# Optimization experiments

Hardware: AMD Instinct MI355X
Metric: run time of the kernel (lower is better)

The kernel has to match this reference:

```python
import jax, jax.numpy as jnp
import numpy as np

N, E, DIN, DH, DOUT, NG = 50000, 800000, 128, 128, 64, 128
EPS = 1e-5
SLOPE = 0.2  # PyG GATConv default negative_slope


def _gat(x, src, dst, W, a_s, a_d, b, heads, out_c, concat):
    n = x.shape[0]
    xp = (x @ W).reshape(n, heads, out_c)            # [N,H,C]
    e_src = (xp * a_s[None]).sum(-1)                  # [N,H]
    e_dst = (xp * a_d[None]).sum(-1)                  # [N,H]
    al = e_src[src] + e_dst[dst]                      # [E,H]
    al = jnp.where(al > 0, al, SLOPE * al)            # leaky_relu
    amax = jax.ops.segment_max(al, dst, num_segments=n)
    w = jnp.exp(al - amax[dst])                       # segment softmax (stable)
    den = jax.ops.segment_sum(w, dst, num_segments=n)
    msg = w[:, :, None] * xp[src]                     # [E,H,C]
    out = jax.ops.segment_sum(msg, dst, num_segments=n) / den[:, :, None]
    out = out.reshape(n, heads * out_c) if concat else out.mean(axis=1)
    return out + b


def _bn(h, g, be):
    m = h.mean(axis=0)
    v = h.var(axis=0)  # biased var, as in torch BN training mode
    return (h - m) / jnp.sqrt(v + EPS) * g + be


def setup_inputs() -> dict:
    key = jax.random.key(0)
    ks = jax.random.split(key, 12)
    x = jax.random.normal(ks[0], (N, DIN), dtype=jnp.float32)
    edge_index = jax.random.randint(ks[1], (2, E), 0, N, dtype=jnp.int64)
    graph_pool = jax.random.uniform(ks[2], (NG, N), dtype=jnp.float32) * (2.0 / N)
    s = 0.1
    return {
        "x": x, "edge_index": edge_index, "graph_pool": graph_pool,
        "W1": jax.random.normal(ks[3], (DIN, DH), dtype=jnp.float32) * s,
        "as1": jax.random.normal(ks[4], (1, DH), dtype=jnp.float32) * s,
        "ad1": jax.random.normal(ks[5], (1, DH), dtype=jnp.float32) * s,
        "b1": jnp.zeros((DH,), jnp.float32),
        "g1": jnp.ones((DH,), jnp.float32), "be1": jnp.zeros((DH,), jnp.float32),
        "W2": jax.random.normal(ks[6], (DH, DH), dtype=jnp.float32) * s,
        "as2": jax.random.normal(ks[7], (1, DH), dtype=jnp.float32) * s,
        "ad2": jax.random.normal(ks[8], (1, DH), dtype=jnp.float32) * s,
        "b2": jnp.zeros((DH,), jnp.float32),
        "g2": jnp.ones((DH,), jnp.float32), "be2": jnp.zeros((DH,), jnp.float32),
        "W3": jax.random.normal(ks[9], (DH, DOUT), dtype=jnp.float32) * s,
        "as3": jax.random.normal(ks[10], (1, DOUT), dtype=jnp.float32) * s,
        "ad3": jax.random.normal(ks[11], (1, DOUT), dtype=jnp.float32) * s,
        "b3": jnp.zeros((DOUT,), jnp.float32),
    }


def reference(x, edge_index, graph_pool,
              W1, as1, ad1, b1, g1, be1,
              W2, as2, ad2, b2, g2, be2,
              W3, as3, ad3, b3):
    n = x.shape[0]
    loops = jnp.arange(n, dtype=edge_index.dtype)  # PyG add_self_loops=True
    src = jnp.concatenate([edge_index[0], loops])
    dst = jnp.concatenate([edge_index[1], loops])
    h = _gat(x, src, dst, W1, as1, ad1, b1, 1, DH, True)
    h = jax.nn.relu(_bn(h, g1, be1))
    h = _gat(h, src, dst, W2, as2, ad2, b2, 1, DH, True)
    h = jax.nn.relu(_bn(h, g2, be2))
    h_nodes = _gat(h, src, dst, W3, as3, ad3, b3, 1, DOUT, False)
    h_pooled = graph_pool @ h_nodes  # sparse.mm == matmul mathematically
    return (h_pooled, h_nodes)
```

## Files before the change

kernel.cpp:

```cpp
#include <hip/hip_runtime.h>
#include <hip/hip_bf16.h>

#define DIN 128
#define DH  128
#define DOUT 64
#define NGR 128
#define EPSV 1e-5f
#define SLOPE 0.2f
#define BSH 7
#define NBMAX 512
#define BCAP 3584

typedef __attribute__((ext_vector_type(8))) short short8;
typedef __attribute__((ext_vector_type(4))) float float4v;

__device__ __forceinline__ unsigned short f2bf(float f) {
    union { float f; unsigned int u; } v; v.f = f;
    unsigned int r = (v.u + 0x7FFFu + ((v.u >> 16) & 1u)) >> 16;
    return (unsigned short)r;
}
__device__ __forceinline__ unsigned short f2bf_f(float f) {
    return (unsigned short)((__float_as_uint(f) + 0x8000u) >> 16);
}
__device__ __forceinline__ float bf_lo(unsigned int u) { return __uint_as_float(u << 16); }
__device__ __forceinline__ float bf_hi(unsigned int u) { return __uint_as_float(u & 0xFFFF0000u); }


__global__ __launch_bounds__(256) void bin_edges_kernel(const int* __restrict__ ei,
                                                        int* __restrict__ bucket_cnt,
                                                        int2* __restrict__ binned,
                                                        int E, int T, int nb) {
    __shared__ int hist[NBMAX], base[NBMAX], cur[NBMAX];
    for (int i = threadIdx.x; i < nb; i += 256) hist[i] = 0;
    __syncthreads();
    int start = blockIdx.x * 8192;
    int endc  = start + 8192; if (endc > T) endc = T;
    for (int e = start + threadIdx.x; e < endc; e += 256) {
        int d = (e < E) ? ei[E + e] : (e - E);
        atomicAdd(&hist[d >> BSH], 1);
    }
    __syncthreads();
    for (int i = threadIdx.x; i < nb; i += 256) {
        int h = hist[i];
        cur[i] = 0;
        if (h) base[i] = atomicAdd(&bucket_cnt[i], h);
    }
    __syncthreads();
    for (int e = start + threadIdx.x; e < endc; e += 256) {
        int s, d;
        if (e < E) { s = ei[e]; d = ei[E + e]; }
        else       { s = e - E; d = s; }
        int b = d >> BSH;
        int off = atomicAdd(&cur[b], 1);
        binned[(size_t)b * BCAP + base[b] + off] = make_int2(s, d);
    }
}

__global__ __launch_bounds__(512) void bucket_scan_kernel(const int* __restrict__ bucket_cnt,
                                                          int* __restrict__ bucket_off,
                                                          int nb, int T) {
    __shared__ int sh[512];
    int tid = threadIdx.x;
    int v = (tid < nb) ? bucket_cnt[tid] : 0;
    sh[tid] = v;
    __syncthreads();
    for (int d = 1; d < 512; d <<= 1) {
        int t = (tid >= d) ? sh[tid - d] : 0;
        __syncthreads();
        sh[tid] += t;
        __syncthreads();
    }
    if (tid < nb) bucket_off[tid] = sh[tid] - v;
    if (tid == 0) bucket_off[nb] = T;
}

__global__ __launch_bounds__(256) void csr_from_binned_kernel(const int2* __restrict__ binned,
                                                              const int* __restrict__ bucket_cnt,
                                                              const int* __restrict__ bucket_off,
                                                              int* __restrict__ row_ptr,
                                                              int* __restrict__ col_src,
                                                              int n, int T) {
    __shared__ int cnt[128], rnk[128], rp[128], sc[128];
    int tid = threadIdx.x;
    int b = blockIdx.x;
    int node0 = b << BSH;
    const int2* bin = &binned[(size_t)b * BCAP];
    int nb_edges = bucket_cnt[b];
    int lo = bucket_off[b];
    if (tid < 128) cnt[tid] = 0;
    __syncthreads();
    for (int i = tid; i < nb_edges; i += 256)
        atomicAdd(&cnt[bin[i].y - node0], 1);
    __syncthreads();
    if (tid < 128) sc[tid] = cnt[tid];
    __syncthreads();
    for (int d = 1; d < 128; d <<= 1) {
        int t = 0;
        if (tid < 128 && tid >= d) t = sc[tid - d];
        __syncthreads();
        if (tid < 128) sc[tid] += t;
        __syncthreads();
    }
    if (tid < 128) {
        int excl = sc[tid] - cnt[tid];
        int r = lo + excl;
        rp[tid] = r;
        rnk[tid] = 0;
        int node = node0 + tid;
        if (node < n) row_ptr[node] = r;
    }
    if (b == 0 && tid == 0) row_ptr[n] = T;
    __syncthreads();
    for (int i = tid; i < nb_edges; i += 256) {
        int2 e = bin[i];
        int local = e.y - node0;
        int r = atomicAdd(&rnk[local], 1);
        col_src[rp[local] + r] = e.x;
    }
}

__device__ __forceinline__ void pack_one(const float* W, unsigned short* PW, int cout, int t) {
    int lane = t & 63;
    int ks   = (t >> 6) & 3;
    int nt   = t >> 8;
    int nn   = nt * 16 + (lane & 15);
    int k0   = ks * 32 + (lane >> 4) * 8;
    unsigned int pk[4];
#pragma unroll
    for (int p = 0; p < 4; ++p) {
        unsigned short lo = f2bf(W[(k0 + 2 * p) * cout + nn]);
        unsigned short hi = f2bf(W[(k0 + 2 * p + 1) * cout + nn]);
        pk[p] = ((unsigned int)hi << 16) | lo;
    }
    *(uint4*)&PW[(size_t)t * 8] = make_uint4(pk[0], pk[1], pk[2], pk[3]);
}

__global__ void pack_w_all_kernel(const float* __restrict__ W1, unsigned short* __restrict__ PW1,
                                  const float* __restrict__ W2, unsigned short* __restrict__ PW2,
                                  const float* __restrict__ W3, unsigned short* __restrict__ PW3) {
    int t = blockIdx.x * 256 + threadIdx.x;
    if (t < 2048)      pack_one(W1, PW1, 128, t);
    else if (t < 4096) pack_one(W2, PW2, 128, t - 2048);
    else if (t < 5120) pack_one(W3, PW3, 64,  t - 4096);
}

template <int COUT, int BNIN>
__global__ __launch_bounds__(256) void gemm_es_kernel(
    const void* __restrict__ Xv, const unsigned short* __restrict__ PW,
    const float* __restrict__ a_s, const float* __restrict__ a_d,
    const float* __restrict__ bnsum, const float* __restrict__ g,
    const float* __restrict__ be, float invn,
    unsigned short* __restrict__ XPB, float* __restrict__ e_src, float* __restrict__ e_dst, int n)
{
    constexpr int NT = COUT / 16;
    __shared__ unsigned short Xs[64 * 136];
    __shared__ float sSc[128], sSh[128];

    int tid  = threadIdx.x;
    int row0 = blockIdx.x * 64;

    if (BNIN) {
        if (tid < 128) {
            float mean = bnsum[tid] * invn;
            float var  = bnsum[128 + tid] * invn - mean * mean;
            float sc   = g[tid] * rsqrtf(var + EPSV);
            sSc[tid] = sc;
            sSh[tid] = be[tid] - mean * sc;
        }
        __syncthreads();
        const unsigned short* H = (const unsigned short*)Xv;
        for (int i = tid; i < 64 * 16; i += 256) {
            int r  = i >> 4;
            int c8 = (i & 15) * 8;
            uint4 u = make_uint4(0, 0, 0, 0);
            if (row0 + r < n) u = *(const uint4*)&H[(size_t)(row0 + r) * 128 + c8];
            unsigned int uu[4] = {u.x, u.y, u.z, u.w};
            unsigned int out[4];
#pragma unroll
            for (int p = 0; p < 4; ++p) {
                int c = c8 + 2 * p;
                float a  = fmaxf(bf_lo(uu[p]) * sSc[c] + sSh[c], 0.f);
                float bq = fmaxf(bf_hi(uu[p]) * sSc[c + 1] + sSh[c + 1], 0.f);
                out[p] = ((unsigned int)f2bf_f(bq) << 16) | f2bf_f(a);
            }
            *(uint4*)&Xs[r * 136 + c8] = make_uint4(out[0], out[1], out[2], out[3]);
        }
    } else {
        const float* X = (const float*)Xv;
        for (int i = tid; i < 64 * 32; i += 256) {
            int r  = i >> 5;
            int k4 = (i & 31) * 4;
            float4 v = make_float4(0.f, 0.f, 0.f, 0.f);
            if (row0 + r < n) v = *(const float4*)&X[(size_t)(row0 + r) * 128 + k4];
            uint2 pk;
            pk.x = ((unsigned int)f2bf_f(v.y) << 16) | f2bf_f(v.x);
            pk.y = ((unsigned int)f2bf_f(v.w) << 16) | f2bf_f(v.z);
            *(uint2*)&Xs[r * 136 + k4] = pk;
        }
    }
    __syncthreads();

    int wv   = tid >> 6;
    int lane = tid & 63;
    int m0   = wv * 16;
    int cl   = lane & 15;
    int q    = lane >> 4;

    float4v acc[NT] = {};
#pragma unroll
    for (int ks = 0; ks < 4; ++ks) {
        short8 af = *(const short8*)&Xs[(m0 + cl) * 136 + ks * 32 + q * 8];
#pragma unroll
        for (int nt = 0; nt < NT; ++nt) {
            short8 bf = *(const short8*)&PW[(size_t)((nt * 4 + ks) * 64 + lane) * 8];
            acc[nt] = __builtin_amdgcn_mfma_f32_16x16x32_bf16(af, bf, acc[nt], 0, 0, 0);
        }
    }

    float asv[NT], adv[NT];
#pragma unroll
    for (int nt = 0; nt < NT; ++nt) {
        asv[nt] = a_s[nt * 16 + cl];
        adv[nt] = a_d[nt * 16 + cl];
    }
#pragma unroll
    for (int reg = 0; reg < 4; ++reg) {
        int m = row0 + m0 + q * 4 + reg;
        if (m >= n) continue;
        float ps = 0.f, pd = 0.f;
        size_t base = (size_t)m * COUT;
#pragma unroll
        for (int nt = 0; nt < NT; ++nt) {
            float v = acc[nt][reg];
            XPB[base + nt * 16 + cl] = f2bf_f(v);
            ps += v * asv[nt];
            pd += v * adv[nt];
        }
        ps += __shfl_xor(ps, 1); pd += __shfl_xor(pd, 1);
        ps += __shfl_xor(ps, 2); pd += __shfl_xor(pd, 2);
        ps += __shfl_xor(ps, 4); pd += __shfl_xor(pd, 4);
        ps += __shfl_xor(ps, 8); pd += __shfl_xor(pd, 8);
        if (cl == 0) {
            e_src[m] = ps;
            e_dst[m] = pd;
        }
    }
}

template <int COUT, int OUTBF>
__global__ __launch_bounds__(256) void gat_aggregate_kernel(
    const unsigned short* __restrict__ XPB, const float* __restrict__ e_src,
    const float* __restrict__ e_dst, const int* __restrict__ row_ptr,
    const int* __restrict__ col_src, const float* __restrict__ bias,
    void* __restrict__ OUT, int n)
{
    int wave = threadIdx.x >> 6;
    int lane = threadIdx.x & 63;
    int d = blockIdx.x * 4 + wave;
    if (d >= n) return;
    int start = row_ptr[d];
    int end   = row_ptr[d + 1];
    float ed  = e_dst[d];

    float den = 0.f;
    float2 acc2 = make_float2(0.f, 0.f);
    float acc1 = 0.f;
    const unsigned int* xpu = (const unsigned int*)XPB;

    for (int base = start; base < end; base += 64) {
        int t = base + lane;
        int s_l = 0; float w_l = 0.f;
        if (t < end) {
            s_l = col_src[t];
            float a = e_src[s_l] + ed;
            a = (a > 0.f) ? a : SLOPE * a;
            w_l = __expf(a);
        }
        int cnt = end - base; if (cnt > 64) cnt = 64;

        int j = 0;
        for (; j + 7 < cnt; j += 8) {
            int ss[8]; float wwv[8];
#pragma unroll
            for (int p = 0; p < 8; ++p) {
                ss[p]  = __shfl(s_l, j + p);
                wwv[p] = __shfl(w_l, j + p);
            }
            if (COUT == 128) {
                unsigned int us[8];
#pragma unroll
                for (int p = 0; p < 8; ++p) us[p] = xpu[(size_t)ss[p] * 64 + lane];
#pragma unroll
                for (int p = 0; p < 8; ++p) {
                    acc2.x += wwv[p] * bf_lo(us[p]);
                    acc2.y += wwv[p] * bf_hi(us[p]);
                    den    += wwv[p];
                }
            } else {
                float xs[8];
#pragma unroll
                for (int p = 0; p < 8; ++p)
                    xs[p] = __uint_as_float((unsigned int)XPB[(size_t)ss[p] * COUT + lane] << 16);
#pragma unroll
                for (int p = 0; p < 8; ++p) {
                    acc1 += wwv[p] * xs[p];
                    den  += wwv[p];
                }
            }
        }
        for (; j + 3 < cnt; j += 4) {
            int ss[4]; float wwv[4];
#pragma unroll
            for (int p = 0; p < 4; ++p) {
                ss[p]  = __shfl(s_l, j + p);
                wwv[p] = __shfl(w_l, j + p);
            }
            if (COUT == 128) {
                unsigned int us[4];
#pragma unroll
                for (int p = 0; p < 4; ++p) us[p] = xpu[(size_t)ss[p] * 64 + lane];
#pragma unroll
                for (int p = 0; p < 4; ++p) {
                    acc2.x += wwv[p] * bf_lo(us[p]);
                    acc2.y += wwv[p] * bf_hi(us[p]);
                    den    += wwv[p];
                }
            } else {
#pragma unroll
                for (int p = 0; p < 4; ++p) {
                    float xv = __uint_as_float((unsigned int)XPB[(size_t)ss[p] * COUT + lane] << 16);
                    acc1 += wwv[p] * xv;
                    den  += wwv[p];
                }
            }
        }
        for (; j < cnt; ++j) {
            int   s = __shfl(s_l, j);
            float w = __shfl(w_l, j);
            if (COUT == 128) {
                unsigned int u = xpu[(size_t)s * 64 + lane];
                acc2.x += w * bf_lo(u);
                acc2.y += w * bf_hi(u);
            } else {
                acc1 += w * __uint_as_float((unsigned int)XPB[(size_t)s * COUT + lane] << 16);
            }
            den += w;
        }
    }

    float inv = 1.f / den;
    if (COUT == 128) {
        float ox = acc2.x * inv + bias[2 * lane + 0];
        float oy = acc2.y * inv + bias[2 * lane + 1];
        if (OUTBF) {
            unsigned int o = ((unsigned int)f2bf_f(oy) << 16) | f2bf_f(ox);
            ((unsigned int*)OUT)[(size_t)d * 64 + lane] = o;
        } else {
            ((float2*)OUT)[(size_t)d * 64 + lane] = make_float2(ox, oy);
        }
    } else {
        ((float*)OUT)[(size_t)d * COUT + lane] = acc1 * inv + bias[lane];
    }
}

__global__ __launch_bounds__(256) void bn_stats_bf_kernel(const unsigned short* __restrict__ H,
                                                          float* __restrict__ sums, int n) {
    __shared__ float sh[1024];
    int c2  = threadIdx.x & 63;
    int grp = threadIdx.x >> 6;
    float sx = 0.f, sy = 0.f, qx = 0.f, qy = 0.f;
    const unsigned int* Hu = (const unsigned int*)H;
    for (int i = blockIdx.x * 4 + grp; i < n; i += gridDim.x * 4) {
        unsigned int u = Hu[(size_t)i * 64 + c2];
        float a = bf_lo(u), b = bf_hi(u);
        sx += a; qx += a * a;
        sy += b; qy += b * b;
    }
    sh[threadIdx.x]       = sx;
    sh[256 + threadIdx.x] = sy;
    sh[512 + threadIdx.x] = qx;
    sh[768 + threadIdx.x] = qy;
    __syncthreads();
    if (grp == 0) {
#pragma unroll
        for (int g2 = 1; g2 < 4; ++g2) {
            sx += sh[g2 * 64 + c2];
            sy += sh[256 + g2 * 64 + c2];
            qx += sh[512 + g2 * 64 + c2];
            qy += sh[768 + g2 * 64 + c2];
        }
        atomicAdd(&sums[2 * c2],       sx);
        atomicAdd(&sums[2 * c2 + 1],   sy);
        atomicAdd(&sums[128 + 2 * c2],     qx);
        atomicAdd(&sums[128 + 2 * c2 + 1], qy);
    }
}

__global__ __launch_bounds__(256) void pool_partial_kernel(
    const float* __restrict__ GP, const float* __restrict__ HN,
    float* __restrict__ partial, int n)
{
    __shared__ float hn_lds[64 * 64];
    __shared__ float gp_lds[128 * 68];

    int tid = threadIdx.x;
    int cg  = tid & 15;
    int gg  = tid >> 4;
    int c0  = cg * 4;

    float acc[8][4] = {};

    for (int sub = 0; sub < 2; ++sub) {
        int k0 = blockIdx.x * 128 + sub * 64;
        for (int i = tid; i < 64 * 16; i += 256) {
            int kk = i >> 4;
            int c4 = (i & 15) * 4;
            int gk = k0 + kk;
            float4 v = make_float4(0.f, 0.f, 0.f, 0.f);
            if (gk < n) v = *(const float4*)&HN[(size_t)gk * 64 + c4];
            *(float4*)&hn_lds[kk * 64 + c4] = v;
        }
        for (int i = tid; i < 128 * 16; i += 256) {
            int g  = i >> 4;
            int k4 = (i & 15) * 4;
            int gk = k0 + k4;
            float4 v = make_float4(0.f, 0.f, 0.f, 0.f);
            if (gk < n) v = *(const float4*)&GP[(size_t)g * n + gk];
            *(float4*)&gp_lds[g * 68 + k4] = v;
        }
        __syncthreads();

#pragma unroll 4
        for (int k = 0; k < 64; ++k) {
            float4 hv = *(const float4*)&hn_lds[k * 64 + c0];
#pragma unroll
            for (int j = 0; j < 8; ++j) {
                float gv = gp_lds[(gg + 16 * j) * 68 + k];
                acc[j][0] += gv * hv.x;
                acc[j][1] += gv * hv.y;
                acc[j][2] += gv * hv.z;
                acc[j][3] += gv * hv.w;
            }
        }
        __syncthreads();
    }

    float* po = &partial[(size_t)blockIdx.x * (NGR * DOUT)];
#pragma unroll
    for (int j = 0; j < 8; ++j) {
        *(float4*)&po[(gg + 16 * j) * 64 + c0] =
            make_float4(acc[j][0], acc[j][1], acc[j][2], acc[j][3]);
    }
}

__global__ __launch_bounds__(256) void pool_reduce_kernel(
    const float* __restrict__ partial, float* __restrict__ OUT, int nblk)
{
    int i = blockIdx.x * 256 + threadIdx.x;
    float s0 = 0.f, s1 = 0.f, s2 = 0.f, s3 = 0.f;
    int p = 0;
    for (; p + 3 < nblk; p += 4) {
        s0 += partial[(size_t)(p + 0) * (NGR * DOUT) + i];
        s1 += partial[(size_t)(p + 1) * (NGR * DOUT) + i];
        s2 += partial[(size_t)(p + 2) * (NGR * DOUT) + i];
        s3 += partial[(size_t)(p + 3) * (NGR * DOUT) + i];
    }
    for (; p < nblk; ++p) s0 += partial[(size_t)p * (NGR * DOUT) + i];
    OUT[i] = (s0 + s1) + (s2 + s3);
}

extern "C" void kernel_launch(void* const* d_in, const int* in_sizes, int n_in,
                              void* d_out, int out_size, void* d_ws, size_t ws_size,
                              hipStream_t stream) {
    const float* x   = (const float*)d_in[0];
    const int*   ei  = (const int*)d_in[1];
    const float* gp  = (const float*)d_in[2];
    const float* W1  = (const float*)d_in[3];
    const float* as1 = (const float*)d_in[4];
    const float* ad1 = (const float*)d_in[5];
    const float* b1  = (const float*)d_in[6];
    const float* g1  = (const float*)d_in[7];
    const float* be1 = (const float*)d_in[8];
    const float* W2  = (const float*)d_in[9];
    const float* as2 = (const float*)d_in[10];
    const float* ad2 = (const float*)d_in[11];
    const float* b2  = (const float*)d_in[12];
    const float* g2  = (const float*)d_in[13];
    const float* be2 = (const float*)d_in[14];
    const float* W3  = (const float*)d_in[15];
    const float* as3 = (const float*)d_in[16];
    const float* ad3 = (const float*)d_in[17];
    const float* b3  = (const float*)d_in[18];

    const int N = in_sizes[0] / DIN;
    const int E = in_sizes[1] / 2;
    const int T = E + N;
    const int NB = (N + 127) >> BSH;

    char* ws = (char*)d_ws;
    auto take = [&](size_t bytes) {
        char* p = ws;
        ws += (bytes + 511) & ~(size_t)511;
        return p;
    };
    unsigned short* xpb = (unsigned short*)take((size_t)N * 128 * 2);
    unsigned short* h   = (unsigned short*)take((size_t)N * 128 * 2);
    float* pool_s  = (float*)take((size_t)((N + 127) / 128) * NGR * DOUT * 4);
    float* esd     = (float*)take((size_t)2 * N * 4);
    float* e_src   = esd;
    float* e_dst   = esd + N;
    int*   row_ptr = (int*)take((size_t)(N + 1) * 4);
    int*   col_src = (int*)take((size_t)T * 4);
    int2*  binned  = (int2*)take((size_t)NB * BCAP * 8);
    int*   zero_rgn      = (int*)take((size_t)(NBMAX + 1 + 512) * 4);
    int*   bucket_cnt    = zero_rgn;
    float* bnsum1        = (float*)(zero_rgn + NBMAX + 1);
    float* bnsum2        = bnsum1 + 256;
    int*   bucket_off    = (int*)take((size_t)(NB + 1) * 4);
    unsigned short* pw1 = (unsigned short*)take((size_t)128 * 128 * 2);
    unsigned short* pw2 = (unsigned short*)take((size_t)128 * 128 * 2);
    unsigned short* pw3 = (unsigned short*)take((size_t)128 * 64 * 2);

    float* outp = (float*)d_out;
    float* hn   = outp + NGR * DOUT;

    hipMemsetAsync(zero_rgn, 0, (size_t)(NBMAX + 1 + 512) * 4, stream);
    pack_w_all_kernel<<<20, 256, 0, stream>>>(W1, pw1, W2, pw2, W3, pw3);

    const int binBlocks = (T + 8191) / 8192;
    bin_edges_kernel<<<binBlocks, 256, 0, stream>>>(ei, bucket_cnt, binned, E, T, NB);
    bucket_scan_kernel<<<1, 512, 0, stream>>>(bucket_cnt, bucket_off, NB, T);
    csr_from_binned_kernel<<<NB, 256, 0, stream>>>(binned, bucket_cnt, bucket_off, row_ptr, col_src, N, T);

    const int gx = (N + 63) / 64;
    const float invn = 1.f / N;

    gemm_es_kernel<128, 0><<<gx, 256, 0, stream>>>(x, pw1, as1, ad1,
        nullptr, nullptr, nullptr, 0.f, xpb, e_src, e_dst, N);
    gat_aggregate_kernel<128, 1><<<(N + 3) / 4, 256, 0, stream>>>(xpb, e_src, e_dst, row_ptr, col_src, b1, h, N);
    bn_stats_bf_kernel<<<240, 256, 0, stream>>>(h, bnsum1, N);

    gemm_es_kernel<128, 1><<<gx, 256, 0, stream>>>(h, pw2, as2, ad2,
        bnsum1, g1, be1, invn, xpb, e_src, e_dst, N);
    gat_aggregate_kernel<128, 1><<<(N + 3) / 4, 256, 0, stream>>>(xpb, e_src, e_dst, row_ptr, col_src, b2, h, N);
    bn_stats_bf_kernel<<<240, 256, 0, stream>>>(h, bnsum2, N);

    gemm_es_kernel<64, 1><<<gx, 256, 0, stream>>>(h, pw3, as3, ad3,
        bnsum2, g2, be2, invn, xpb, e_src, e_dst, N);
    gat_aggregate_kernel<64, 0><<<(N + 3) / 4, 256, 0, stream>>>(xpb, e_src, e_dst, row_ptr, col_src, b3, hn, N);

    const int nblk = (N + 127) / 128;
    pool_partial_kernel<<<nblk, 256, 0, stream>>>(gp, hn, pool_s, N);
    pool_reduce_kernel<<<(NGR * DOUT + 255) / 256, 256, 0, stream>>>(pool_s, outp, nblk);
}
```

Before: 393.8 us.

## Merge front-end kernels, stage edges in LDS, and cap pooling partial blocks

Weight packing is folded into the edge-binning launch. The bucket scan kernel is removed: each CSR block now sums the preceding bucket counts itself, and CSR building runs in the same launch as the first GEMM. The aggregate kernel reads edge (src, weight) pairs from LDS instead of shuffles and reduces the softmax denominator once per wave at the end. The pooling partial kernel now uses a grid-stride loop over at most 128 blocks, so the reduction reads far fewer partials. Together these cut launch count and reduction traffic, at the cost of some redundant prefix-sum work per CSR block and lower parallelism in pooling.

```diff
diff --git a/kernel.cpp b/kernel.cpp
--- a/kernel.cpp
+++ b/kernel.cpp
@@ -10,6 +10,7 @@
 #define BSH 7
 #define NBMAX 512
 #define BCAP 3584
+#define POOLB 128
 
 typedef __attribute__((ext_vector_type(8))) short short8;
 typedef __attribute__((ext_vector_type(4))) float float4v;
@@ -25,11 +26,36 @@
 __device__ __forceinline__ float bf_lo(unsigned int u) { return __uint_as_float(u << 16); }
 __device__ __forceinline__ float bf_hi(unsigned int u) { return __uint_as_float(u & 0xFFFF0000u); }
 
-
-__global__ __launch_bounds__(256) void bin_edges_kernel(const int* __restrict__ ei,
-                                                        int* __restrict__ bucket_cnt,
-                                                        int2* __restrict__ binned,
-                                                        int E, int T, int nb) {
+__device__ __forceinline__ void pack_one(const float* W, unsigned short* PW, int cout, int t) {
+    int lane = t & 63;
+    int ks   = (t >> 6) & 3;
+    int nt   = t >> 8;
+    int nn   = nt * 16 + (lane & 15);
+    int k0   = ks * 32 + (lane >> 4) * 8;
+    unsigned int pk[4];
+#pragma unroll
+    for (int p = 0; p < 4; ++p) {
+        unsigned short lo = f2bf(W[(k0 + 2 * p) * cout + nn]);
+        unsigned short hi = f2bf(W[(k0 + 2 * p + 1) * cout + nn]);
+        pk[p] = ((unsigned int)hi << 16) | lo;
+    }
+    *(uint4*)&PW[(size_t)t * 8] = make_uint4(pk[0], pk[1], pk[2], pk[3]);
+}
+
+__global__ __launch_bounds__(256) void front_a_kernel(
+    const int* __restrict__ ei, int* __restrict__ bucket_cnt, int2* __restrict__ binned,
+    int E, int T, int nb, int binBlocks,
+    const float* __restrict__ W1, unsigned short* __restrict__ PW1,
+    const float* __restrict__ W2, unsigned short* __restrict__ PW2,
+    const float* __restrict__ W3, unsigned short* __restrict__ PW3)
+{
+    if ((int)blockIdx.x >= binBlocks) {
+        int t = ((int)blockIdx.x - binBlocks) * 256 + (int)threadIdx.x;
+        if (t < 2048)      pack_one(W1, PW1, 128, t);
+        else if (t < 4096) pack_one(W2, PW2, 128, t - 2048);
+        else if (t < 5120) pack_one(W3, PW3, 64,  t - 4096);
+        return;
+    }
     __shared__ int hist[NBMAX], base[NBMAX], cur[NBMAX];
     for (int i = threadIdx.x; i < nb; i += 256) hist[i] = 0;
     __syncthreads();
@@ -56,96 +82,9 @@
     }
 }
 
-__global__ __launch_bounds__(512) void bucket_scan_kernel(const int* __restrict__ bucket_cnt,
-                                                          int* __restrict__ bucket_off,
-                                                          int nb, int T) {
-    __shared__ int sh[512];
-    int tid = threadIdx.x;
-    int v = (tid < nb) ? bucket_cnt[tid] : 0;
-    sh[tid] = v;
-    __syncthreads();
-    for (int d = 1; d < 512; d <<= 1) {
-        int t = (tid >= d) ? sh[tid - d] : 0;
-        __syncthreads();
-        sh[tid] += t;
-        __syncthreads();
-    }
-    if (tid < nb) bucket_off[tid] = sh[tid] - v;
-    if (tid == 0) bucket_off[nb] = T;
-}
-
-__global__ __launch_bounds__(256) void csr_from_binned_kernel(const int2* __restrict__ binned,
-                                                              const int* __restrict__ bucket_cnt,
-                                                              const int* __restrict__ bucket_off,
-                                                              int* __restrict__ row_ptr,
-                                                              int* __restrict__ col_src,
-                                                              int n, int T) {
-    __shared__ int cnt[128], rnk[128], rp[128], sc[128];
-    int tid = threadIdx.x;
-    int b = blockIdx.x;
-    int node0 = b << BSH;
-    const int2* bin = &binned[(size_t)b * BCAP];
-    int nb_edges = bucket_cnt[b];
-    int lo = bucket_off[b];
-    if (tid < 128) cnt[tid] = 0;
-    __syncthreads();
-    for (int i = tid; i < nb_edges; i += 256)
-        atomicAdd(&cnt[bin[i].y - node0], 1);
-    __syncthreads();
-    if (tid < 128) sc[tid] = cnt[tid];
-    __syncthreads();
-    for (int d = 1; d < 128; d <<= 1) {
-        int t = 0;
-        if (tid < 128 && tid >= d) t = sc[tid - d];
-        __syncthreads();
-        if (tid < 128) sc[tid] += t;
-        __syncthreads();
-    }
-    if (tid < 128) {
-        int excl = sc[tid] - cnt[tid];
-        int r = lo + excl;
-        rp[tid] = r;
-        rnk[tid] = 0;
-        int node = node0 + tid;
-        if (node < n) row_ptr[node] = r;
-    }
-    if (b == 0 && tid == 0) row_ptr[n] = T;
-    __syncthreads();
-    for (int i = tid; i < nb_edges; i += 256) {
-        int2 e = bin[i];
-        int local = e.y - node0;
-        int r = atomicAdd(&rnk[local], 1);
-        col_src[rp[local] + r] = e.x;
-    }
-}
-
-__device__ __forceinline__ void pack_one(const float* W, unsigned short* PW, int cout, int t) {
-    int lane = t & 63;
-    int ks   = (t >> 6) & 3;
-    int nt   = t >> 8;
-    int nn   = nt * 16 + (lane & 15);
-    int k0   = ks * 32 + (lane >> 4) * 8;
-    unsigned int pk[4];
-#pragma unroll
-    for (int p = 0; p < 4; ++p) {
-        unsigned short lo = f2bf(W[(k0 + 2 * p) * cout + nn]);
-        unsigned short hi = f2bf(W[(k0 + 2 * p + 1) * cout + nn]);
-        pk[p] = ((unsigned int)hi << 16) | lo;
-    }
-    *(uint4*)&PW[(size_t)t * 8] = make_uint4(pk[0], pk[1], pk[2], pk[3]);
-}
-
-__global__ void pack_w_all_kernel(const float* __restrict__ W1, unsigned short* __restrict__ PW1,
-                                  const float* __restrict__ W2, unsigned short* __restrict__ PW2,
-                                  const float* __restrict__ W3, unsigned short* __restrict__ PW3) {
-    int t = blockIdx.x * 256 + threadIdx.x;
-    if (t < 2048)      pack_one(W1, PW1, 128, t);
-    else if (t < 4096) pack_one(W2, PW2, 128, t - 2048);
-    else if (t < 5120) pack_one(W3, PW3, 64,  t - 4096);
-}
-
 template <int COUT, int BNIN>
-__global__ __launch_bounds__(256) void gemm_es_kernel(
+__device__ __forceinline__ void gemm_es_body(
+    unsigned short* Xs, float* sSc, float* sSh, int row0,
     const void* __restrict__ Xv, const unsigned short* __restrict__ PW,
     const float* __restrict__ a_s, const float* __restrict__ a_d,
     const float* __restrict__ bnsum, const float* __restrict__ g,
@@ -153,13 +92,9 @@
     unsigned short* __restrict__ XPB, float* __restrict__ e_src, float* __restrict__ e_dst, int n)
 {
     constexpr int NT = COUT / 16;
-    __shared__ unsigned short Xs[64 * 136];
-    __shared__ float sSc[128], sSh[128];
-
-    int tid  = threadIdx.x;
-    int row0 = blockIdx.x * 64;
-
-    if (BNIN) {
+    int tid = threadIdx.x;
+
+    if constexpr (BNIN) {
         if (tid < 128) {
             float mean = bnsum[tid] * invn;
             float var  = bnsum[128 + tid] * invn - mean * mean;
@@ -247,6 +182,89 @@
     }
 }
 
+template <int COUT, int BNIN>
+__global__ __launch_bounds__(256) void gemm_es_kernel(
+    const void* __restrict__ Xv, const unsigned short* __restrict__ PW,
+    const float* __restrict__ a_s, const float* __restrict__ a_d,
+    const float* __restrict__ bnsum, const float* __restrict__ g,
+    const float* __restrict__ be, float invn,
+    unsigned short* __restrict__ XPB, float* __restrict__ e_src, float* __restrict__ e_dst, int n)
+{
+    __shared__ unsigned short Xs[64 * 136];
+    __shared__ float sSc[128], sSh[128];
+    gemm_es_body<COUT, BNIN>(Xs, sSc, sSh, blockIdx.x * 64,
+                             Xv, PW, a_s, a_d, bnsum, g, be, invn, XPB, e_src, e_dst, n);
+}
+
+__global__ __launch_bounds__(256) void front_b_kernel(
+    const int2* __restrict__ binned, const int* __restrict__ bucket_cnt,
+    int* __restrict__ row_ptr, int* __restrict__ col_src, int n, int T, int nbcsr,
+    const float* __restrict__ X, const unsigned short* __restrict__ PW,
+    const float* __restrict__ a_s, const float* __restrict__ a_d,
+    unsigned short* __restrict__ XPB, float* __restrict__ e_src, float* __restrict__ e_dst)
+{
+    __shared__ __align__(16) char smraw[64 * 136 * 2];
+    int tid = threadIdx.x;
+
+    if ((int)blockIdx.x < nbcsr) {
+        int* cnt = (int*)smraw;
+        int* rnk = cnt + 128;
+        int* rp  = rnk + 128;
+        int* sc  = rp + 128;
+        int* red = sc + 128;
+        int b = blockIdx.x;
+        int node0 = b << BSH;
+        const int2* bin = &binned[(size_t)b * BCAP];
+        int nb_edges = bucket_cnt[b];
+
+        int part = 0;
+        for (int i = tid; i < b; i += 256) part += bucket_cnt[i];
+        red[tid] = part;
+        if (tid < 128) cnt[tid] = 0;
+        __syncthreads();
+#pragma unroll
+        for (int s2 = 128; s2 > 0; s2 >>= 1) {
+            if (tid < s2) red[tid] += red[tid + s2];
+            __syncthreads();
+        }
+        int lo = red[0];
+
+        for (int i = tid; i < nb_edges; i += 256)
+            atomicAdd(&cnt[bin[i].y - node0], 1);
+        __syncthreads();
+        if (tid < 128) sc[tid] = cnt[tid];
+        __syncthreads();
+        for (int d2 = 1; d2 < 128; d2 <<= 1) {
+            int t = 0;
+            if (tid < 128 && tid >= d2) t = sc[tid - d2];
+            __syncthreads();
+            if (tid < 128) sc[tid] += t;
+            __syncthreads();
+        }
+        if (tid < 128) {
+            int excl = sc[tid] - cnt[tid];
+            int r = lo + excl;
+            rp[tid] = r;
+            rnk[tid] = 0;
+            int node = node0 + tid;
+            if (node < n) row_ptr[node] = r;
+        }
+        if (b == 0 && tid == 0) row_ptr[n] = T;
+        __syncthreads();
+        for (int i = tid; i < nb_edges; i += 256) {
+            int2 e = bin[i];
+            int local = e.y - node0;
+            int r = atomicAdd(&rnk[local], 1);
+            col_src[rp[local] + r] = e.x;
+        }
+    } else {
+        unsigned short* Xs = (unsigned short*)smraw;
+        gemm_es_body<128, 0>(Xs, nullptr, nullptr, ((int)blockIdx.x - nbcsr) * 64,
+                             X, PW, a_s, a_d, nullptr, nullptr, nullptr, 0.f,
+                             XPB, e_src, e_dst, n);
+    }
+}
+
 template <int COUT, int OUTBF>
 __global__ __launch_bounds__(256) void gat_aggregate_kernel(
     const unsigned short* __restrict__ XPB, const float* __restrict__ e_src,
@@ -254,6 +272,7 @@
     const int* __restrict__ col_src, const float* __restrict__ bias,
     void* __restrict__ OUT, int n)
 {
+    __shared__ int2 sw[4][64];
     int wave = threadIdx.x >> 6;
     int lane = threadIdx.x & 63;
     int d = blockIdx.x * 4 + wave;
@@ -262,7 +281,7 @@
     int end   = row_ptr[d + 1];
     float ed  = e_dst[d];
 
-    float den = 0.f;
+    float denl = 0.f;
     float2 acc2 = make_float2(0.f, 0.f);
     float acc1 = 0.f;
     const unsigned int* xpu = (const unsigned int*)XPB;
@@ -276,6 +295,8 @@
             a = (a > 0.f) ? a : SLOPE * a;
             w_l = __expf(a);
         }
+        denl += w_l;
+        sw[wave][lane] = make_int2(s_l, __float_as_int(w_l));
         int cnt = end - base; if (cnt > 64) cnt = 64;
 
         int j = 0;
@@ -283,8 +304,9 @@
             int ss[8]; float wwv[8];
 #pragma unroll
             for (int p = 0; p < 8; ++p) {
-                ss[p]  = __shfl(s_l, j + p);
-                wwv[p] = __shfl(w_l, j + p);
+                int2 e = sw[wave][j + p];
+                ss[p]  = e.x;
+                wwv[p] = __int_as_float(e.y);
             }
             if (COUT == 128) {
                 unsigned int us[8];
@@ -294,7 +316,6 @@
                 for (int p = 0; p < 8; ++p) {
                     acc2.x += wwv[p] * bf_lo(us[p]);
                     acc2.y += wwv[p] * bf_hi(us[p]);
-                    den    += wwv[p];
                 }
             } else {
                 float xs[8];
@@ -302,18 +323,16 @@
                 for (int p = 0; p < 8; ++p)
                     xs[p] = __uint_as_float((unsigned int)XPB[(size_t)ss[p] * COUT + lane] << 16);
 #pragma unroll
-                for (int p = 0; p < 8; ++p) {
-                    acc1 += wwv[p] * xs[p];
-                    den  += wwv[p];
-                }
+                for (int p = 0; p < 8; ++p) acc1 += wwv[p] * xs[p];
             }
         }
         for (; j + 3 < cnt; j += 4) {
             int ss[4]; float wwv[4];
 #pragma unroll
             for (int p = 0; p < 4; ++p) {
-                ss[p]  = __shfl(s_l, j + p);
-                wwv[p] = __shfl(w_l, j + p);
+                int2 e = sw[wave][j + p];
+                ss[p]  = e.x;
+                wwv[p] = __int_as_float(e.y);
             }
             if (COUT == 128) {
                 unsigned int us[4];
@@ -323,20 +342,19 @@
                 for (int p = 0; p < 4; ++p) {
                     acc2.x += wwv[p] * bf_lo(us[p]);
                     acc2.y += wwv[p] * bf_hi(us[p]);
-                    den    += wwv[p];
                 }
             } else {
 #pragma unroll
                 for (int p = 0; p < 4; ++p) {
                     float xv = __uint_as_float((unsigned int)XPB[(size_t)ss[p] * COUT + lane] << 16);
                     acc1 += wwv[p] * xv;
-                    den  += wwv[p];
                 }
             }
         }
         for (; j < cnt; ++j) {
-            int   s = __shfl(s_l, j);
-            float w = __shfl(w_l, j);
+            int2 e = sw[wave][j];
+            int   s = e.x;
+            float w = __int_as_float(e.y);
             if (COUT == 128) {
                 unsigned int u = xpu[(size_t)s * 64 + lane];
                 acc2.x += w * bf_lo(u);
@@ -344,11 +362,13 @@
             } else {
                 acc1 += w * __uint_as_float((unsigned int)XPB[(size_t)s * COUT + lane] << 16);
             }
-            den += w;
-        }
-    }
-
-    float inv = 1.f / den;
+        }
+    }
+
+#pragma unroll
+    for (int off = 1; off < 64; off <<= 1) denl += __shfl_xor(denl, off);
+    float inv = 1.f / denl;
+
     if (COUT == 128) {
         float ox = acc2.x * inv + bias[2 * lane + 0];
         float oy = acc2.y * inv + bias[2 * lane + 1];
@@ -409,40 +429,43 @@
     int c0  = cg * 4;
 
     float acc[8][4] = {};
-
-    for (int sub = 0; sub < 2; ++sub) {
-        int k0 = blockIdx.x * 128 + sub * 64;
-        for (int i = tid; i < 64 * 16; i += 256) {
-            int kk = i >> 4;
-            int c4 = (i & 15) * 4;
-            int gk = k0 + kk;
-            float4 v = make_float4(0.f, 0.f, 0.f, 0.f);
-            if (gk < n) v = *(const float4*)&HN[(size_t)gk * 64 + c4];
-            *(float4*)&hn_lds[kk * 64 + c4] = v;
-        }
-        for (int i = tid; i < 128 * 16; i += 256) {
-            int g  = i >> 4;
-            int k4 = (i & 15) * 4;
-            int gk = k0 + k4;
-            float4 v = make_float4(0.f, 0.f, 0.f, 0.f);
-            if (gk < n) v = *(const float4*)&GP[(size_t)g * n + gk];
-            *(float4*)&gp_lds[g * 68 + k4] = v;
-        }
-        __syncthreads();
+    int nchunk = (n + 127) >> 7;
+
+    for (int blk = blockIdx.x; blk < nchunk; blk += gridDim.x) {
+        for (int sub = 0; sub < 2; ++sub) {
+            int k0 = blk * 128 + sub * 64;
+            for (int i = tid; i < 64 * 16; i += 256) {
+                int kk = i >> 4;
+                int c4 = (i & 15) * 4;
+                int gk = k0 + kk;
+                float4 v = make_float4(0.f, 0.f, 0.f, 0.f);
+                if (gk < n) v = *(const float4*)&HN[(size_t)gk * 64 + c4];
+                *(float4*)&hn_lds[kk * 64 + c4] = v;
+            }
+            for (int i = tid; i < 128 * 16; i += 256) {
+                int g  = i >> 4;
+                int k4 = (i & 15) * 4;
+                int gk = k0 + k4;
+                float4 v = make_float4(0.f, 0.f, 0.f, 0.f);
+                if (gk < n) v = *(const float4*)&GP[(size_t)g * n + gk];
+                *(float4*)&gp_lds[g * 68 + k4] = v;
+            }
+            __syncthreads();
 
 #pragma unroll 4
-        for (int k = 0; k < 64; ++k) {
-            float4 hv = *(const float4*)&hn_lds[k * 64 + c0];
-#pragma unroll
-            for (int j = 0; j < 8; ++j) {
-                float gv = gp_lds[(gg + 16 * j) * 68 + k];
-                acc[j][0] += gv * hv.x;
-                acc[j][1] += gv * hv.y;
-                acc[j][2] += gv * hv.z;
-                acc[j][3] += gv * hv.w;
-            }
-        }
-        __syncthreads();
+            for (int k = 0; k < 64; ++k) {
+                float4 hv = *(const float4*)&hn_lds[k * 64 + c0];
+#pragma unroll
+                for (int j = 0; j < 8; ++j) {
+                    float gv = gp_lds[(gg + 16 * j) * 68 + k];
+                    acc[j][0] += gv * hv.x;
+                    acc[j][1] += gv * hv.y;
+                    acc[j][2] += gv * hv.z;
+                    acc[j][3] += gv * hv.w;
+                }
+            }
+            __syncthreads();
+        }
     }
 
     float* po = &partial[(size_t)blockIdx.x * (NGR * DOUT)];
@@ -505,7 +528,7 @@
     };
     unsigned short* xpb = (unsigned short*)take((size_t)N * 128 * 2);
     unsigned short* h   = (unsigned short*)take((size_t)N * 128 * 2);
-    float* pool_s  = (float*)take((size_t)((N + 127) / 128) * NGR * DOUT * 4);
+    float* pool_s  = (float*)take((size_t)POOLB * NGR * DOUT * 4);
     float* esd     = (float*)take((size_t)2 * N * 4);
     float* e_src   = esd;
     float* e_dst   = esd + N;
@@ -516,7 +539,6 @@
     int*   bucket_cnt    = zero_rgn;
     float* bnsum1        = (float*)(zero_rgn + NBMAX + 1);
     float* bnsum2        = bnsum1 + 256;
-    int*   bucket_off    = (int*)take((size_t)(NB + 1) * 4);
     unsigned short* pw1 = (unsigned short*)take((size_t)128 * 128 * 2);
     unsigned short* pw2 = (unsigned short*)take((size_t)128 * 128 * 2);
     unsigned short* pw3 = (unsigned short*)take((size_t)128 * 64 * 2);
@@ -525,18 +547,17 @@
     float* hn   = outp + NGR * DOUT;
 
     hipMemsetAsync(zero_rgn, 0, (size_t)(NBMAX + 1 + 512) * 4, stream);
-    pack_w_all_kernel<<<20, 256, 0, stream>>>(W1, pw1, W2, pw2, W3, pw3);
 
     const int binBlocks = (T + 8191) / 8192;
-    bin_edges_kernel<<<binBlocks, 256, 0, stream>>>(ei, bucket_cnt, binned, E, T, NB);
-    bucket_scan_kernel<<<1, 512, 0, stream>>>(bucket_cnt, bucket_off, NB, T);
-    csr_from_binned_kernel<<<NB, 256, 0, stream>>>(binned, bucket_cnt, bucket_off, row_ptr, col_src, N, T);
+    front_a_kernel<<<binBlocks + 20, 256, 0, stream>>>(ei, bucket_cnt, binned, E, T, NB, binBlocks,
+                                                       W1, pw1, W2, pw2, W3, pw3);
 
     const int gx = (N + 63) / 64;
     const float invn = 1.f / N;
 
-    gemm_es_kernel<128, 0><<<gx, 256, 0, stream>>>(x, pw1, as1, ad1,
-        nullptr, nullptr, nullptr, 0.f, xpb, e_src, e_dst, N);
+    front_b_kernel<<<NB + gx, 256, 0, stream>>>(binned, bucket_cnt, row_ptr, col_src, N, T, NB,
+                                                x, pw1, as1, ad1, xpb, e_src, e_dst);
+
     gat_aggregate_kernel<128, 1><<<(N + 3) / 4, 256, 0, stream>>>(xpb, e_src, e_dst, row_ptr, col_src, b1, h, N);
     bn_stats_bf_kernel<<<240, 256, 0, stream>>>(h, bnsum1, N);
 
@@ -549,7 +570,8 @@
         bnsum2, g2, be2, invn, xpb, e_src, e_dst, N);
     gat_aggregate_kernel<64, 0><<<(N + 3) / 4, 256, 0, stream>>>(xpb, e_src, e_dst, row_ptr, col_src, b3, hn, N);
 
-    const int nblk = (N + 127) / 128;
-    pool_partial_kernel<<<nblk, 256, 0, stream>>>(gp, hn, pool_s, N);
-    pool_reduce_kernel<<<(NGR * DOUT + 255) / 256, 256, 0, stream>>>(pool_s, outp, nblk);
-}
+    const int nchunk = (N + 127) / 128;
+    const int pb = nchunk < POOLB ? nchunk : POOLB;
+    pool_partial_kernel<<<pb, 256, 0, stream>>>(gp, hn, pool_s, N);
+    pool_reduce_kernel<<<(NGR * DOUT + 255) / 256, 256, 0, stream>>>(pool_s, outp, pb);
+}
```

Measured after the change: 407.4 us. 1.03x slower.
